# Performance work log

Measured on AMD Instinct MI355X. Metric: run time of the kernel, lower is better.

The kernel has to match this reference:

```python
import jax, jax.numpy as jnp
import numpy as np

KERNEL_SIZE = 16
STRIDE = 8
NEG = -1.0e9


def setup_inputs() -> dict:
    key = jax.random.key(0)
    k1, k2, k3, k4, k5 = jax.random.split(key, 5)
    B, C, L = 8, 512, 4096
    x = jax.random.normal(k1, (B, C, L), dtype=jnp.float32)
    mask = jax.random.randint(k2, (B, L), 0, 2).astype(bool)
    W = jax.random.normal(k3, (C, C), dtype=jnp.float32) * 0.02
    b = jax.random.normal(k4, (C,), dtype=jnp.float32) * 0.02
    v = jax.random.normal(k5, (C,), dtype=jnp.float32) * 0.02
    return {"x": x, "mask": mask, "W": W, "b": b, "v": v}


def reference(x, mask, W, b, v):
    # x: [B, C, L], mask: [B, L] (True = masked out)
    B, C, L = x.shape
    win, step = KERNEL_SIZE, STRIDE
    L_pool = 1 + (L - win) // step
    # per-token projection (identical across windows since proj is per-token)
    h = jnp.tanh(jnp.einsum('bcl,dc->bld', x, W) + b)      # [B, L, C]
    s = jnp.einsum('bld,d->bl', h, v)                       # [B, L]
    idx = jnp.arange(L_pool)[:, None] * step + jnp.arange(win)[None, :]
    sw = s[:, idx]
    mw = mask[:, idx]
    sw = jnp.where(mw, NEG, sw)
    w = jax.nn.softmax(sw, axis=-1)
    w = jnp.where(mw, 0.0, w)
    norm = jnp.clip(jnp.sum(w, axis=-1, keepdims=True), 1e-6, None)
    w = w / norm
    xw = x[:, :, idx]
    return jnp.einsum('bcpw,bpw->bcp', xw, w)               # [B, C, L_pool]
```

## Files before the change

### kernel.cpp

```cpp
#include <hip/hip_runtime.h>
#include <hip/hip_bf16.h>
#include <cmath>

#define Bsz 8
#define Csz 512
#define Lsz 4096
#define LPOOL 511
#define NEGV -1000000000.0f

typedef __attribute__((ext_vector_type(8))) short short8;
typedef __attribute__((ext_vector_type(4))) float float4v;

__device__ __forceinline__ float bf2f(short u) {
  unsigned int x = ((unsigned int)(unsigned short)u) << 16;
  return __builtin_bit_cast(float, x);
}

__device__ __forceinline__ float ftanh(float x) {
  float e = __expf(2.0f * x);
  return 1.0f - 2.0f * __builtin_amdgcn_rcpf(e + 1.0f);
}

__global__ __launch_bounds__(256) void prep(const unsigned char* __restrict__ mb,
    int* __restrict__ flag, const float* __restrict__ W,
    __hip_bfloat16* __restrict__ Wts) {
  const int tid = threadIdx.x;
  const int pb = blockIdx.x;
  if (pb == 0) {
    __shared__ int sf;
    if (tid == 0) sf = 0;
    __syncthreads();
    int f = 0;
    for (int i = tid; i < 4096; i += 256)
      if ((i & 3) && mb[i]) f = 1;
    if (f) atomicOr(&sf, 1);
    __syncthreads();
    if (tid == 0) *flag = sf;
  } else {
    int tg = (pb - 1) * 256 + tid;
    int d = tg >> 6, cg = tg & 63;
    float4 w0 = *(const float4*)(W + (size_t)d * 512 + cg * 8);
    float4 w1 = *(const float4*)(W + (size_t)d * 512 + cg * 8 + 4);
    __hip_bfloat16 hb[8];
    hb[0] = __float2bfloat16(w0.x); hb[1] = __float2bfloat16(w0.y);
    hb[2] = __float2bfloat16(w0.z); hb[3] = __float2bfloat16(w0.w);
    hb[4] = __float2bfloat16(w1.x); hb[5] = __float2bfloat16(w1.y);
    hb[6] = __float2bfloat16(w1.z); hb[7] = __float2bfloat16(w1.w);
    int nt = d >> 7, row = d & 127, ks = cg >> 2, seg = cg & 3;
    *(short8*)(Wts + (((size_t)nt * 16 + ks) * 512 + seg * 128 + row) * 8) = *(short8*)hb;
  }
}

__global__ __launch_bounds__(256, 2) void gemm_fused(
    const float* __restrict__ x, const __hip_bfloat16* __restrict__ Wts,
    const float* __restrict__ bias, const float* __restrict__ v,
    float* __restrict__ s) {
  __shared__ short8 sA[4096];
  __shared__ float sXw4[4][672];

  const int tid = threadIdx.x;
  const int lane = tid & 63, wave = tid >> 6;
  const int mt = blockIdx.x;
  const int b = mt >> 6;
  const int l0 = (mt & 63) << 6;

  {
    float* sXw = sXw4[wave];
    const int r = lane >> 1;
    const int q = lane & 1;
    const int ll = lane & 15, ks2 = lane >> 4;
    const float* xg = x + (((size_t)(b * Csz + r)) << 12) + (size_t)(l0 + wave * 16 + q * 8);

    float4 A0a = *(const float4*)(xg);
    float4 A0b = *(const float4*)(xg + 4);
    float4 A1a = *(const float4*)(xg + (1u << 17));
    float4 A1b = *(const float4*)(xg + (1u << 17) + 4);
    float4 A2a = *(const float4*)(xg + (2u << 17));
    float4 A2b = *(const float4*)(xg + (2u << 17) + 4);

    #pragma unroll
    for (int cc = 0; cc < 16; ++cc) {
      float4 Na = A2a, Nb = A2b;
      if (cc < 13) {
        const float* xn = xg + ((size_t)(cc + 3) << 17);
        Na = *(const float4*)(xn);
        Nb = *(const float4*)(xn + 4);
      }
      float* wp = &sXw[r * 21 + q * 8];
      wp[0] = A0a.x; wp[1] = A0a.y; wp[2] = A0a.z; wp[3] = A0a.w;
      wp[4] = A0b.x; wp[5] = A0b.y; wp[6] = A0b.z; wp[7] = A0b.w;
      float tv[8];
      #pragma unroll
      for (int j = 0; j < 8; ++j) tv[j] = sXw[(ks2 * 8 + j) * 21 + ll];
      __hip_bfloat16 ab[8];
      #pragma unroll
      for (int j = 0; j < 8; ++j) ab[j] = __float2bfloat16(tv[j]);
      sA[(cc * 4 + ks2) * 64 + wave * 16 + ll] = *(short8*)ab;
      A0a = A1a; A0b = A1b; A1a = A2a; A1b = A2b; A2a = Na; A2b = Nb;
    }
  }

  const int lr = lane & 15, quad = lane >> 4;
  const int mh = wave >> 1, nh = wave & 1;

  __syncthreads();

  const short8* Bp = (const short8*)Wts + quad * 128 + nh * 64 + lr;
#define LDB(dst, idx)                                                          \
  {                                                                            \
    const short8* bp = Bp + ((size_t)(idx) << 9);                              \
    dst[0] = bp[0]; dst[1] = bp[16]; dst[2] = bp[32]; dst[3] = bp[48];         \
  }
  short8 bq[4][4];
  LDB(bq[0], 0) LDB(bq[1], 1) LDB(bq[2], 2) LDB(bq[3], 3)

  float sp[2][4];
  #pragma unroll
  for (int mf = 0; mf < 2; ++mf)
    #pragma unroll
    for (int reg = 0; reg < 4; ++reg) sp[mf][reg] = 0.f;

  #pragma unroll
  for (int nt = 0; nt < 4; ++nt) {
    float bl[4], vl[4];
    #pragma unroll
    for (int nf = 0; nf < 4; ++nf) {
      int n = nt * 128 + nh * 64 + nf * 16 + lr;
      bl[nf] = bias[n];
      vl[nf] = v[n];
    }
    float4v acc[2][4];
    #pragma unroll
    for (int mf = 0; mf < 2; ++mf)
      #pragma unroll
      for (int nf = 0; nf < 4; ++nf) acc[mf][nf] = (float4v)0.f;

    #pragma unroll
    for (int ks = 0; ks < 16; ++ks) {
      const int idx = nt * 16 + ks;
      short8 af[2];
      af[0] = sA[(ks * 4 + quad) * 64 + mh * 32 + lr];
      af[1] = sA[(ks * 4 + quad) * 64 + mh * 32 + 16 + lr];
      __builtin_amdgcn_s_setprio(1);
      #pragma unroll
      for (int mf = 0; mf < 2; ++mf)
        #pragma unroll
        for (int nf = 0; nf < 4; ++nf)
          acc[mf][nf] = __builtin_amdgcn_mfma_f32_16x16x32_bf16(
              af[mf], bq[idx & 3][nf], acc[mf][nf], 0, 0, 0);
      __builtin_amdgcn_s_setprio(0);
      if (idx + 4 < 64) LDB(bq[idx & 3], idx + 4)
    }
    #pragma unroll
    for (int mf = 0; mf < 2; ++mf)
      #pragma unroll
      for (int reg = 0; reg < 4; ++reg) {
        float pp = 0.f;
        #pragma unroll
        for (int nf = 0; nf < 4; ++nf)
          pp += ftanh(acc[mf][nf][reg] + bl[nf]) * vl[nf];
        sp[mf][reg] += pp;
      }
  }
#undef LDB

  float* sRed = (float*)sXw4;
  float pv[2][4];
  #pragma unroll
  for (int mf = 0; mf < 2; ++mf)
    #pragma unroll
    for (int reg = 0; reg < 4; ++reg) {
      float p = sp[mf][reg];
      p += __shfl_xor(p, 1, 16);
      p += __shfl_xor(p, 2, 16);
      p += __shfl_xor(p, 4, 16);
      p += __shfl_xor(p, 8, 16);
      pv[mf][reg] = p;
    }
  __syncthreads();
  if (nh == 1 && lr == 0) {
    #pragma unroll
    for (int mf = 0; mf < 2; ++mf)
      #pragma unroll
      for (int reg = 0; reg < 4; ++reg)
        sRed[((mh * 2 + mf) * 4 + quad) * 4 + reg] = pv[mf][reg];
  }
  __syncthreads();
  if (nh == 0 && lr == 0) {
    #pragma unroll
    for (int mf = 0; mf < 2; ++mf)
      #pragma unroll
      for (int reg = 0; reg < 4; ++reg)
        s[mt * 64 + mh * 32 + mf * 16 + quad * 4 + reg] =
            pv[mf][reg] + sRed[((mh * 2 + mf) * 4 + quad) * 4 + reg];
  }
}

__global__ void win_weights(const float* __restrict__ s, const void* __restrict__ mask,
                            const int* __restrict__ flag, float* __restrict__ wgt) {
  int t = blockIdx.x * blockDim.x + threadIdx.x;
  if (t >= Bsz * LPOOL) return;
  int b = t / LPOOL, p = t - b * LPOOL;
  const bool u8 = (*flag != 0);
  const unsigned char* m8 = (const unsigned char*)mask;
  const int* m32 = (const int*)mask;
  float sv[16]; int mv[16];
  float mx = -3.4e38f;
  int base = b * Lsz + p * 8;
  #pragma unroll
  for (int w = 0; w < 16; ++w) {
    int mk = u8 ? (int)m8[base + w] : m32[base + w];
    float val = mk ? NEGV : s[base + w];
    sv[w] = val; mv[w] = mk;
    mx = fmaxf(mx, val);
  }
  float sum = 0.f;
  #pragma unroll
  for (int w = 0; w < 16; ++w) { sv[w] = expf(sv[w] - mx); sum += sv[w]; }
  float inv = 1.0f / sum;
  float norm = 0.f;
  #pragma unroll
  for (int w = 0; w < 16; ++w) { sv[w] = mv[w] ? 0.f : sv[w] * inv; norm += sv[w]; }
  norm = fmaxf(norm, 1e-6f);
  float rn = 1.0f / norm;
  #pragma unroll
  for (int w = 0; w < 16; ++w) wgt[t * 16 + w] = sv[w] * rn;
}

__global__ __launch_bounds__(256) void pool_out(const float* __restrict__ x,
    const float* __restrict__ wgt, float* __restrict__ out) {
  __shared__ float xrow[Lsz];
  int bc = blockIdx.x;
  int c = bc & (Csz - 1);
  int b = bc >> 9;
  const float* xr = x + ((size_t)b * Csz + c) * Lsz;
  int tid = threadIdx.x;
  #pragma unroll
  for (int it = 0; it < 4; ++it) {
    int idx = (tid + it * 256) << 2;
    *(float4*)(&xrow[idx]) = *(const float4*)(&xr[idx]);
  }
  __syncthreads();
  const float* wb = wgt + (size_t)b * LPOOL * 16;
  float* ob = out + ((size_t)b * Csz + c) * LPOOL;
  for (int p = tid; p < LPOOL; p += 256) {
    const float4* wp = (const float4*)(wb + p * 16);
    const float4* xp = (const float4*)(&xrow[p * 8]);
    float acc = 0.f;
    #pragma unroll
    for (int q = 0; q < 4; ++q) {
      float4 wv = wp[q], xv = xp[q];
      acc += xv.x * wv.x + xv.y * wv.y + xv.z * wv.z + xv.w * wv.w;
    }
    ob[p] = acc;
  }
}

__global__ void detect_mask(const unsigned char* __restrict__ mb, int* __restrict__ flag) {
  __shared__ int sf;
  int t = threadIdx.x;
  if (t == 0) sf = 0;
  __syncthreads();
  int f = 0;
  for (int i = t; i < 4096; i += 256)
    if ((i & 3) && mb[i]) f = 1;
  if (f) atomicOr(&sf, 1);
  __syncthreads();
  if (t == 0) *flag = sf;
}

__global__ __launch_bounds__(256) void gemm_s_f32(const float* __restrict__ x,
    const float* __restrict__ W, const float* __restrict__ bias,
    const float* __restrict__ v, float* __restrict__ s_out) {
  __shared__ float sA[32][64];
  __shared__ float sB[32][68];
  __shared__ float s_acc[64];
  const int tid = threadIdx.x;
  const int b = blockIdx.y;
  const int l0 = blockIdx.x * 64;
  if (tid < 64) s_acc[tid] = 0.0f;
  const int tx = tid & 15;
  const int ty = tid >> 4;
  const float* xb = x + ((size_t)b * Csz) * Lsz + l0;
  for (int d0 = 0; d0 < Csz; d0 += 64) {
    float acc[4][4] = {{0.f}};
    for (int c0 = 0; c0 < Csz; c0 += 32) {
      __syncthreads();
      #pragma unroll
      for (int it = 0; it < 8; ++it) {
        int idx = tid + it * 256;
        int kc = idx >> 6, ml = idx & 63;
        sA[kc][ml] = xb[(size_t)(c0 + kc) * Lsz + ml];
      }
      #pragma unroll
      for (int it = 0; it < 8; ++it) {
        int idx = tid + it * 256;
        int kc = idx & 31, dj = idx >> 5;
        sB[kc][dj] = W[(size_t)(d0 + dj) * Csz + c0 + kc];
      }
      __syncthreads();
      #pragma unroll
      for (int kc = 0; kc < 32; ++kc) {
        float4 a  = *(const float4*)(&sA[kc][tx << 2]);
        float4 w4 = *(const float4*)(&sB[kc][ty << 2]);
        acc[0][0] += a.x * w4.x; acc[0][1] += a.x * w4.y; acc[0][2] += a.x * w4.z; acc[0][3] += a.x * w4.w;
        acc[1][0] += a.y * w4.x; acc[1][1] += a.y * w4.y; acc[1][2] += a.y * w4.z; acc[1][3] += a.y * w4.w;
        acc[2][0] += a.z * w4.x; acc[2][1] += a.z * w4.y; acc[2][2] += a.z * w4.z; acc[2][3] += a.z * w4.w;
        acc[3][0] += a.w * w4.x; acc[3][1] += a.w * w4.y; acc[3][2] += a.w * w4.z; acc[3][3] += a.w * w4.w;
      }
    }
    float part[4] = {0.f, 0.f, 0.f, 0.f};
    #pragma unroll
    for (int j = 0; j < 4; ++j) {
      int d = d0 + (ty << 2) + j;
      float bj = bias[d], vj = v[d];
      #pragma unroll
      for (int i = 0; i < 4; ++i)
        part[i] += tanhf(acc[i][j] + bj) * vj;
    }
    #pragma unroll
    for (int i = 0; i < 4; ++i)
      atomicAdd(&s_acc[(tx << 2) + i], part[i]);
  }
  __syncthreads();
  if (tid < 64) s_out[(size_t)b * Lsz + l0 + tid] = s_acc[tid];
}

extern "C" void kernel_launch(void* const* d_in, const int* in_sizes, int n_in,
                              void* d_out, int out_size, void* d_ws, size_t ws_size,
                              hipStream_t stream) {
  const float* x    = (const float*)d_in[0];
  const void*  mask = d_in[1];
  const float* W    = (const float*)d_in[2];
  const float* bias = (const float*)d_in[3];
  const float* v    = (const float*)d_in[4];
  float* out = (float*)d_out;

  char* wsb = (char*)d_ws;
  int*   flag = (int*)wsb;
  float* s    = (float*)(wsb + 256);
  float* wgt  = (float*)(wsb + 131328);
  __hip_bfloat16* Wts = (__hip_bfloat16*)(wsb + 393216);
  const size_t NEED = 917504;

  if (ws_size >= NEED) {
    prep<<<129, 256, 0, stream>>>((const unsigned char*)mask, flag, W, Wts);
    gemm_fused<<<512, 256, 0, stream>>>(x, Wts, bias, v, s);
    win_weights<<<(Bsz * LPOOL + 255) / 256, 256, 0, stream>>>(s, mask, flag, wgt);
    pool_out<<<Bsz * Csz, 256, 0, stream>>>(x, wgt, out);
  } else {
    detect_mask<<<1, 256, 0, stream>>>((const unsigned char*)mask, flag);
    gemm_s_f32<<<dim3(Lsz / 64, Bsz), 256, 0, stream>>>(x, W, bias, v, s);
    win_weights<<<(Bsz * LPOOL + 255) / 256, 256, 0, stream>>>(s, mask, flag, wgt);
    pool_out<<<Bsz * Csz, 256, 0, stream>>>(x, wgt, out);
  }
}
```

Measured before the change: 147.0 us.

## Fuse window-weight softmax into pooling kernel with double-buffered channel rows

Replaces the separate win_weights and pool_out kernels with a single pool3 kernel. Each block recomputes the window softmax weights for its batch into shared memory, then processes 8 channels, prefetching the next channel row into registers while it computes the current one. This removes one launch and the global round-trip of the weights, and amortizes weight loading over 8 channels. In exchange, the weight computation is repeated 64 times per batch, and the large shared-memory footprint (about 66 KB) plus only 512 blocks limits occupancy.

```diff
diff --git a/kernel.cpp b/kernel.cpp
--- a/kernel.cpp
+++ b/kernel.cpp
@@ -196,6 +196,97 @@
   }
 }
 
+__global__ __launch_bounds__(256) void pool3(const float* __restrict__ x,
+    const float* __restrict__ s, const void* __restrict__ mask,
+    const int* __restrict__ flag, float* __restrict__ out) {
+  __shared__ float wl[LPOOL][17];
+  __shared__ float xrow[2][Lsz];
+  const int t = threadIdx.x;
+  const int c0 = blockIdx.x * 8, b = blockIdx.y;
+
+  {
+    const float* xr = x + ((size_t)(b * Csz + c0)) * Lsz;
+    #pragma unroll
+    for (int it = 0; it < 4; ++it) {
+      int idx = (t + it * 256) * 4;
+      *(float4*)(&xrow[0][idx]) = *(const float4*)(xr + idx);
+    }
+  }
+  {
+    const bool u8 = (*flag != 0);
+    const unsigned char* m8 = (const unsigned char*)mask;
+    const int* m32 = (const int*)mask;
+    for (int p = t; p < LPOOL; p += 256) {
+      const int base = b * Lsz + p * 8;
+      float sv[16]; int mv[16];
+      float mx = -3.4e38f;
+      #pragma unroll
+      for (int w = 0; w < 16; ++w) {
+        int mk = u8 ? (int)m8[base + w] : m32[base + w];
+        float val = mk ? NEGV : s[base + w];
+        sv[w] = val; mv[w] = mk;
+        mx = fmaxf(mx, val);
+      }
+      float sum = 0.f;
+      #pragma unroll
+      for (int w = 0; w < 16; ++w) { sv[w] = expf(sv[w] - mx); sum += sv[w]; }
+      float inv = 1.0f / sum;
+      float norm = 0.f;
+      #pragma unroll
+      for (int w = 0; w < 16; ++w) { sv[w] = mv[w] ? 0.f : sv[w] * inv; norm += sv[w]; }
+      norm = fmaxf(norm, 1e-6f);
+      float rn = 1.0f / norm;
+      #pragma unroll
+      for (int w = 0; w < 16; ++w) wl[p][w] = sv[w] * rn;
+    }
+  }
+  __syncthreads();
+
+  int cur = 0;
+  for (int cr = 0; cr < 8; ++cr) {
+    const int c = c0 + cr;
+    float4 r0, r1, r2, r3;
+    if (cr < 7) {
+      const float* xn = x + ((size_t)(b * Csz + c + 1)) * Lsz + t * 4;
+      r0 = *(const float4*)(xn);
+      r1 = *(const float4*)(xn + 1024);
+      r2 = *(const float4*)(xn + 2048);
+      r3 = *(const float4*)(xn + 3072);
+    }
+    float* ob = out + ((size_t)(b * Csz + c)) * LPOOL;
+    for (int p = t; p < LPOOL; p += 256) {
+      const float* wp = &wl[p][0];
+      const float* xp = &xrow[cur][p * 8];
+      float acc = 0.f;
+      #pragma unroll
+      for (int qq = 0; qq < 16; ++qq) acc += xp[qq] * wp[qq];
+      ob[p] = acc;
+    }
+    if (cr < 7) {
+      float* xw = &xrow[cur ^ 1][t * 4];
+      *(float4*)(xw)        = r0;
+      *(float4*)(xw + 1024) = r1;
+      *(float4*)(xw + 2048) = r2;
+      *(float4*)(xw + 3072) = r3;
+      __syncthreads();
+      cur ^= 1;
+    }
+  }
+}
+
+__global__ void detect_mask(const unsigned char* __restrict__ mb, int* __restrict__ flag) {
+  __shared__ int sf;
+  int t = threadIdx.x;
+  if (t == 0) sf = 0;
+  __syncthreads();
+  int f = 0;
+  for (int i = t; i < 4096; i += 256)
+    if ((i & 3) && mb[i]) f = 1;
+  if (f) atomicOr(&sf, 1);
+  __syncthreads();
+  if (t == 0) *flag = sf;
+}
+
 __global__ void win_weights(const float* __restrict__ s, const void* __restrict__ mask,
                             const int* __restrict__ flag, float* __restrict__ wgt) {
   int t = blockIdx.x * blockDim.x + threadIdx.x;
@@ -254,19 +345,6 @@
     }
     ob[p] = acc;
   }
-}
-
-__global__ void detect_mask(const unsigned char* __restrict__ mb, int* __restrict__ flag) {
-  __shared__ int sf;
-  int t = threadIdx.x;
-  if (t == 0) sf = 0;
-  __syncthreads();
-  int f = 0;
-  for (int i = t; i < 4096; i += 256)
-    if ((i & 3) && mb[i]) f = 1;
-  if (f) atomicOr(&sf, 1);
-  __syncthreads();
-  if (t == 0) *flag = sf;
 }
 
 __global__ __launch_bounds__(256) void gemm_s_f32(const float* __restrict__ x,
@@ -346,8 +424,7 @@
   if (ws_size >= NEED) {
     prep<<<129, 256, 0, stream>>>((const unsigned char*)mask, flag, W, Wts);
     gemm_fused<<<512, 256, 0, stream>>>(x, Wts, bias, v, s);
-    win_weights<<<(Bsz * LPOOL + 255) / 256, 256, 0, stream>>>(s, mask, flag, wgt);
-    pool_out<<<Bsz * Csz, 256, 0, stream>>>(x, wgt, out);
+    pool3<<<dim3(64, Bsz), 256, 0, stream>>>(x, s, mask, flag, out);
   } else {
     detect_mask<<<1, 256, 0, stream>>>((const unsigned char*)mask, flag);
     gemm_s_f32<<<dim3(Lsz / 64, Bsz), 256, 0, stream>>>(x, W, bias, v, s);
```

Result: no change. 149.4 us (+1.6%).
